# Kernel optimization log

Hardware: AMD Instinct MI355X
Metric: run time of the kernel (lower is better)

Reference implementation:

```python
import jax, jax.numpy as jnp
import numpy as np

NUM_HEADS = 4
NUM_GROUPS = 32
EPS = 1e-5


def setup_inputs() -> dict:
    key = jax.random.key(0)
    ks = jax.random.split(key, 4)
    ch = 256
    x = jax.random.normal(ks[0], (16, ch, 32, 32), dtype=jnp.float32)
    gn_w = jnp.ones((ch,), jnp.float32)
    gn_b = jnp.zeros((ch,), jnp.float32)
    # conv1x1 weights, kaiming-ish scale
    qkv_w = jax.random.normal(ks[1], (3 * ch, ch), dtype=jnp.float32) / np.sqrt(ch)
    qkv_b = jnp.zeros((3 * ch,), jnp.float32)
    proj_w = jax.random.normal(ks[2], (ch, ch), dtype=jnp.float32) / np.sqrt(ch)
    proj_b = jnp.zeros((ch,), jnp.float32)
    return {"x": x, "gn_w": gn_w, "gn_b": gn_b, "qkv_w": qkv_w,
            "qkv_b": qkv_b, "proj_w": proj_w, "proj_b": proj_b}


def _group_norm(x, w, b):
    bsz, c, h, wd = x.shape
    g = NUM_GROUPS
    xg = x.reshape(bsz, g, c // g, h, wd)
    mean = xg.mean(axis=(2, 3, 4), keepdims=True)
    var = xg.var(axis=(2, 3, 4), keepdims=True)
    xg = (xg - mean) * jax.lax.rsqrt(var + EPS)
    return xg.reshape(bsz, c, h, wd) * w[None, :, None, None] + b[None, :, None, None]


def reference(x, gn_w, gn_b, qkv_w, qkv_b, proj_w, proj_b):
    b, c, h, w = x.shape
    hd = c // NUM_HEADS
    scale = hd ** (-0.5)
    y = _group_norm(x, gn_w, gn_b)
    # 1x1 conv == channel matmul
    qkv = jnp.einsum('oc,bchw->bohw', qkv_w, y) + qkv_b[None, :, None, None]
    q, k, v = jnp.split(qkv, 3, axis=1)
    q = q.reshape(b, NUM_HEADS, hd, h * w)
    k = k.reshape(b, NUM_HEADS, hd, h * w)
    v = v.reshape(b, NUM_HEADS, hd, h * w)
    attn = jnp.einsum('bhdi,bhdj->bhij', q * scale, k)
    attn = jax.nn.softmax(attn, axis=-1)
    out = jnp.einsum('bhij,bhdj->bhdi', attn, v)
    out = out.reshape(b, c, h, w)
    out = jnp.einsum('oc,bchw->bohw', proj_w, out) + proj_b[None, :, None, None]
    return x + out
```

## Files before the change

kernel.cpp:

```cpp
#include <hip/hip_runtime.h>
#include <cstddef>

#define B_   16
#define C_   256
#define HW_  1024
#define NH_  4
#define NG_  32
#define CPG_ 8
#define CS_  0.18033688f

typedef __attribute__((ext_vector_type(8))) short bf16x8;
typedef __attribute__((ext_vector_type(4))) short s16x4;
typedef __attribute__((ext_vector_type(8))) _Float16 f16x8;
typedef __attribute__((ext_vector_type(4))) float f32x4;

#define MFMA16B(a, b, c) __builtin_amdgcn_mfma_f32_16x16x32_bf16(a, b, c, 0, 0, 0)
#define MFMA16H(a, b, c) __builtin_amdgcn_mfma_f32_16x16x32_f16(a, b, c, 0, 0, 0)

#if __has_builtin(__builtin_amdgcn_mfma_f32_16x16x16bf16_1k)
#define HAVE_MFMA16K16 1
#define MFMA16B4(a, b, c) __builtin_amdgcn_mfma_f32_16x16x16bf16_1k(a, b, c, 0, 0, 0)
#else
#define HAVE_MFMA16K16 0
#endif

__device__ __forceinline__ float bf2f(unsigned short h) {
    unsigned int u = ((unsigned int)h) << 16;
    return __builtin_bit_cast(float, u);
}
__device__ __forceinline__ unsigned short f2bf(float f) {
    unsigned int u = __builtin_bit_cast(unsigned int, f);
    u += 0x7FFFu + ((u >> 16) & 1u);
    return (unsigned short)(u >> 16);
}
__device__ __forceinline__ unsigned packbf(float a, float b) {
    unsigned ua = __builtin_bit_cast(unsigned, a) + 0x8000u;
    unsigned ub = __builtin_bit_cast(unsigned, b) + 0x8000u;
    return __builtin_amdgcn_perm(ub, ua, 0x07060302u);
}
__device__ __forceinline__ unsigned pkh(float a, float b) {
    auto h2 = __builtin_amdgcn_cvt_pkrtz(a, b);
    return __builtin_bit_cast(unsigned, h2);
}

__global__ __launch_bounds__(256) void wcvt_kernel(
    const float* __restrict__ qw, const float* __restrict__ pw,
    unsigned short* __restrict__ oq, unsigned short* __restrict__ op)
{
    int i = blockIdx.x * 256 + threadIdx.x;
    const float* s; unsigned short* d; int j;
    if (i < 49152) { s = qw; d = oq; j = i; }
    else           { s = pw; d = op; j = i - 49152; }
    float4 f = ((const float4*)s)[j];
    uint2 u = {pkh(f.x, f.y), pkh(f.z, f.w)};
    *(uint2*)&d[(size_t)j * 4] = u;
}

__global__ __launch_bounds__(256) void gn_kernel(
    const float* __restrict__ x,
    const float* __restrict__ gw,
    const float* __restrict__ gb,
    float2* __restrict__ scsh)
{
    int blk = blockIdx.x;
    const float* xg = x + (size_t)blk * CPG_ * HW_;
    const int N = CPG_ * HW_;

    float s = 0.f, ss = 0.f;
    for (int e = threadIdx.x * 4; e < N; e += 1024) {
        float4 v4 = *(const float4*)&xg[e];
        s  += v4.x + v4.y + v4.z + v4.w;
        ss += v4.x * v4.x + v4.y * v4.y + v4.z * v4.z + v4.w * v4.w;
    }
    #pragma unroll
    for (int off = 32; off > 0; off >>= 1) {
        s  += __shfl_down(s, off, 64);
        ss += __shfl_down(ss, off, 64);
    }
    __shared__ float red[8];
    __shared__ float2 stf;
    int lane = threadIdx.x & 63, wv = threadIdx.x >> 6;
    if (lane == 0) { red[wv] = s; red[4 + wv] = ss; }
    __syncthreads();
    if (threadIdx.x == 0) {
        float S  = red[0] + red[1] + red[2] + red[3];
        float SS = red[4] + red[5] + red[6] + red[7];
        float mean = S / (float)N;
        float var  = SS / (float)N - mean * mean;
        stf = make_float2(mean, rsqrtf(var + 1e-5f));
    }
    __syncthreads();
    if (threadIdx.x < 8) {
        int ch = (blk & 31) * CPG_ + threadIdx.x;
        float sc = stf.y * gw[ch];
        float sh = gb[ch] - stf.x * sc;
        scsh[blk * 8 + threadIdx.x] = make_float2(sc, sh);
    }
}

template <bool FUSE_GN, bool FINAL>
__global__ __launch_bounds__(256) void gemm_mfma_kernel(
    const unsigned short* __restrict__ W16,
    const float* __restrict__ Xf,
    const unsigned short* __restrict__ OP,
    const float* __restrict__ LPp,
    const float* __restrict__ bias,
    const float2* __restrict__ scsh,
    const float* __restrict__ res,
    float* __restrict__ outF,
    unsigned short* __restrict__ qT,
    unsigned short* __restrict__ kT,
    unsigned short* __restrict__ vN,
    int M, int K, int N)
{
    __shared__ union {
        struct { unsigned short A[2][128][40]; unsigned short Bt[2][64][40]; } st;
        unsigned short nd[2][64][72];
        unsigned short mn[128][72];
    } L;

    const int b  = blockIdx.z;
    const int m0 = blockIdx.y * 128, n0 = blockIdx.x * 64;
    const int t  = threadIdx.x;
    const int l15 = t & 15, quad = (t >> 4) & 3;
    const int wave = t >> 6, wm = wave >> 1, wn = wave & 1;

    union HF { uint4 q; f16x8 v; };

    f32x4 acc[4][2];
    #pragma unroll
    for (int mt = 0; mt < 4; ++mt)
        #pragma unroll
        for (int nt = 0; nt < 2; ++nt)
            acc[mt][nt] = (f32x4){0.f, 0.f, 0.f, 0.f};

    const int ar = t >> 1, akh = (t & 1) * 16;
    const int bn = t & 63, bkb = t >> 6;

    float rinv[4];
    if (FINAL) {
        int n = n0 + bn;
        #pragma unroll
        for (int h = 0; h < 4; ++h) {
            float l0 = LPp[(size_t)(b * 4 + h) * 1024 + n];
            float l1 = LPp[(size_t)(64 + b * 4 + h) * 1024 + n];
            rinv[h] = 1.f / (l0 + l1);
        }
    }

    uint4 pa0, pa1;
    float pv[8];
    unsigned short ph0[8], ph1[8];
    int   pH = 0;
    float2 ss[8];

    auto PREF = [&](int k0) {
        const unsigned short* wp = &W16[(size_t)(m0 + ar) * K + k0 + akh];
        pa0 = *(const uint4*)wp;
        pa1 = *(const uint4*)(wp + 8);
        int ch = k0 + bkb * 8;
        if (FINAL) {
            pH = ch >> 6;
            size_t base = ((size_t)(b * 4 + pH) * 64 + (ch & 63)) * 1024 + n0 + bn;
            #pragma unroll
            for (int j = 0; j < 8; ++j) {
                ph0[j] = OP[base + (size_t)j * 1024];
                ph1[j] = OP[(size_t)64 * 64 * 1024 + base + (size_t)j * 1024];
            }
        } else {
            const float* xp = &Xf[((size_t)b * K + ch) * N + n0 + bn];
            #pragma unroll
            for (int j = 0; j < 8; ++j) pv[j] = xp[(size_t)j * N];
            if (FUSE_GN) {
                const float4* sp = (const float4*)&scsh[b * C_ + ch];
                #pragma unroll
                for (int q2 = 0; q2 < 4; ++q2) ((float4*)ss)[q2] = sp[q2];
            }
        }
    };

    PREF(0);
    const int NIT = K / 32;
    for (int it = 0; it < NIT; ++it) {
        const int bsel = it & 1;
        *(uint4*)&L.st.A[bsel][ar][akh]     = pa0;
        *(uint4*)&L.st.A[bsel][ar][akh + 8] = pa1;
        {
            float v[8];
            if (FINAL) {
                float ri = rinv[pH];
                #pragma unroll
                for (int j = 0; j < 8; ++j)
                    v[j] = (bf2f(ph0[j]) + bf2f(ph1[j])) * ri;
            } else {
                #pragma unroll
                for (int j = 0; j < 8; ++j) v[j] = pv[j];
                if (FUSE_GN) {
                    #pragma unroll
                    for (int j = 0; j < 8; ++j) v[j] = v[j] * ss[j].x + ss[j].y;
                }
            }
            uint4 bw = {pkh(v[0], v[1]), pkh(v[2], v[3]), pkh(v[4], v[5]), pkh(v[6], v[7])};
            *(uint4*)&L.st.Bt[bsel][bn][bkb * 8] = bw;
        }
        __syncthreads();
        if (it + 1 < NIT) PREF((it + 1) * 32);
        HF af[4], bfv[2];
        #pragma unroll
        for (int mt = 0; mt < 4; ++mt)
            af[mt].q = *(const uint4*)&L.st.A[bsel][wm * 64 + mt * 16 + l15][quad * 8];
        #pragma unroll
        for (int nt = 0; nt < 2; ++nt)
            bfv[nt].q = *(const uint4*)&L.st.Bt[bsel][wn * 32 + nt * 16 + l15][quad * 8];
        #pragma unroll
        for (int mt = 0; mt < 4; ++mt)
            #pragma unroll
            for (int nt = 0; nt < 2; ++nt)
                acc[mt][nt] = MFMA16H(af[mt].v, bfv[nt].v, acc[mt][nt]);
    }
    __syncthreads();

    if (FINAL) {
        #pragma unroll
        for (int mt = 0; mt < 4; ++mt) {
            #pragma unroll
            for (int rr = 0; rr < 4; ++rr) {
                int m = m0 + wm * 64 + mt * 16 + quad * 4 + rr;
                float bv = bias[m];
                #pragma unroll
                for (int nt = 0; nt < 2; ++nt) {
                    int n = n0 + wn * 32 + nt * 16 + l15;
                    size_t off = ((size_t)b * M + m) * (size_t)N + n;
                    outF[off] = acc[mt][nt][rr] + bv + res[off];
                }
            }
        }
    } else if (m0 < 512) {
        const float qsc = (m0 < 256) ? CS_ : 1.f;
        #pragma unroll
        for (int mt = 0; mt < 4; ++mt)
            #pragma unroll
            for (int rr = 0; rr < 4; ++rr) {
                int dl = mt * 16 + quad * 4 + rr;
                float bv = bias[m0 + wm * 64 + dl];
                #pragma unroll
                for (int nt = 0; nt < 2; ++nt)
                    L.nd[wm][wn * 32 + nt * 16 + l15][dl] = f2bf((acc[mt][nt][rr] + bv) * qsc);
            }
        __syncthreads();
        unsigned short* dst = (m0 < 256) ? qT : kT;
        int headbase = (m0 & 255) >> 6;
        int hl = t >> 7, tt = t & 127;
        int nl = tt >> 1, db = (tt & 1) * 32;
        const unsigned short* src = &L.nd[hl][nl][db];
        unsigned short* gp = &dst[(((size_t)(b * 4 + headbase + hl)) * 1024 + n0 + nl) * 64 + db];
        uint4 u0 = *(const uint4*)(src);
        uint4 u1 = *(const uint4*)(src + 8);
        uint4 u2 = *(const uint4*)(src + 16);
        uint4 u3 = *(const uint4*)(src + 24);
        *(uint4*)(gp)      = u0;
        *(uint4*)(gp + 8)  = u1;
        *(uint4*)(gp + 16) = u2;
        *(uint4*)(gp + 24) = u3;
    } else {
        #pragma unroll
        for (int mt = 0; mt < 4; ++mt)
            #pragma unroll
            for (int rr = 0; rr < 4; ++rr) {
                int ml = wm * 64 + mt * 16 + quad * 4 + rr;
                float bv = bias[m0 + ml];
                #pragma unroll
                for (int nt = 0; nt < 2; ++nt)
                    L.mn[ml][wn * 32 + nt * 16 + l15] = f2bf(acc[mt][nt][rr] + bv);
            }
        __syncthreads();
        int ml = t & 127, nb = t >> 7;
        const unsigned short* src = &L.mn[ml][nb * 32];
        unsigned short* gp = &vN[((size_t)b * 256 + (m0 - 512) + ml) * 1024 + n0 + nb * 32];
        uint4 u0 = *(const uint4*)(src);
        uint4 u1 = *(const uint4*)(src + 8);
        uint4 u2 = *(const uint4*)(src + 16);
        uint4 u3 = *(const uint4*)(src + 24);
        *(uint4*)(gp)      = u0;
        *(uint4*)(gp + 8)  = u1;
        *(uint4*)(gp + 16) = u2;
        *(uint4*)(gp + 24) = u3;
    }
}

__global__ __launch_bounds__(256) void attn_mfma_kernel(
    const unsigned short* __restrict__ qT,
    const unsigned short* __restrict__ kT,
    const unsigned short* __restrict__ vN,
    unsigned short* __restrict__ OP,
    float* __restrict__ LP)
{
    __shared__ unsigned short Kt[2][64][72];
    __shared__ unsigned short Vs[2][64][72];

    const int t    = threadIdx.x;
    const int wv   = t >> 6;
    const int l15  = t & 15;
    const int quad = (t >> 4) & 3;
    const int bh   = blockIdx.x;
    const int i0   = blockIdx.y * 128;
    const int jh   = blockIdx.z;

    union FragU { uint4 q; unsigned u[4]; bf16x8 v; };

    FragU qf[2][2];
    {
        const unsigned short* qg = qT + (size_t)bh * (1024 * 64);
        int qrow = i0 + wv * 32 + l15;
        #pragma unroll
        for (int nt = 0; nt < 2; ++nt)
            #pragma unroll
            for (int kt = 0; kt < 2; ++kt)
                qf[nt][kt].q = *(const uint4*)&qg[(size_t)(qrow + nt * 16) * 64 + kt * 32 + quad * 8];
    }

    f32x4 accO[4][2];
    #pragma unroll
    for (int m = 0; m < 4; ++m)
        #pragma unroll
        for (int n = 0; n < 2; ++n)
            accO[m][n] = (f32x4){0.f, 0.f, 0.f, 0.f};
    float l_i[2] = {0.f, 0.f};
#if HAVE_MFMA16K16
    f32x4 accL[2] = {(f32x4){0.f, 0.f, 0.f, 0.f}, (f32x4){0.f, 0.f, 0.f, 0.f}};
    const s16x4 ones4 = {(short)0x3F80, (short)0x3F80, (short)0x3F80, (short)0x3F80};
#endif

    const unsigned short* kg = kT + (size_t)bh * (1024 * 64);
    const unsigned short* vg = vN + (size_t)bh * (64 * 1024);

    const int slbase = l15 + ((quad & 1) << 5);
    const bool upper = (t & 32) != 0;
    (void)slbase; (void)upper;
    const int sr = t >> 2, sc = (t & 3) * 16;

    uint4 kr0, kr1, vr0, vr1;
    {
        const int j0 = jh * 512;
        const unsigned short* kp = &kg[(size_t)(j0 + sr) * 64 + sc];
        const unsigned short* vp = &vg[(size_t)sr * 1024 + j0 + sc];
        kr0 = *(const uint4*)kp;  kr1 = *(const uint4*)(kp + 8);
        vr0 = *(const uint4*)vp;  vr1 = *(const uint4*)(vp + 8);
    }

    for (int it = 0; it < 8; ++it) {
        const int bsel = it & 1;
        *(uint4*)&Kt[bsel][sr][sc]     = kr0;
        *(uint4*)&Kt[bsel][sr][sc + 8] = kr1;
        *(uint4*)&Vs[bsel][sr][sc]     = vr0;
        *(uint4*)&Vs[bsel][sr][sc + 8] = vr1;
        __syncthreads();
        if (it < 7) {
            const int j0n = jh * 512 + (it + 1) * 64;
            const unsigned short* kp = &kg[(size_t)(j0n + sr) * 64 + sc];
            const unsigned short* vp = &vg[(size_t)sr * 1024 + j0n + sc];
            kr0 = *(const uint4*)kp;  kr1 = *(const uint4*)(kp + 8);
            vr0 = *(const uint4*)vp;  vr1 = *(const uint4*)(vp + 8);
        }

        f32x4 accS[4][2];
        #pragma unroll
        for (int mt = 0; mt < 4; ++mt) {
            FragU ak[2];
            #pragma unroll
            for (int kt = 0; kt < 2; ++kt)
                ak[kt].q = *(const uint4*)&Kt[bsel][mt * 16 + l15][kt * 32 + quad * 8];
            #pragma unroll
            for (int nt = 0; nt < 2; ++nt) {
                f32x4 z = (f32x4){0.f, 0.f, 0.f, 0.f};
                z = MFMA16B(ak[0].v, qf[nt][0].v, z);
                z = MFMA16B(ak[1].v, qf[nt][1].v, z);
                accS[mt][nt] = z;
            }
        }

#if HAVE_MFMA16K16
        union PB { unsigned u[2]; s16x4 v; };
        PB pb[4][2];
        #pragma unroll
        for (int mt = 0; mt < 4; ++mt)
            #pragma unroll
            for (int nt = 0; nt < 2; ++nt) {
                float p0 = exp2f(accS[mt][nt][0]);
                float p1 = exp2f(accS[mt][nt][1]);
                float p2 = exp2f(accS[mt][nt][2]);
                float p3 = exp2f(accS[mt][nt][3]);
                pb[mt][nt].u[0] = packbf(p0, p1);
                pb[mt][nt].u[1] = packbf(p2, p3);
            }
        #pragma unroll
        for (int mt = 0; mt < 4; ++mt)
            #pragma unroll
            for (int nt = 0; nt < 2; ++nt)
                accL[nt] = MFMA16B4(ones4, pb[mt][nt].v, accL[nt]);
        #pragma unroll
        for (int mtd = 0; mtd < 4; ++mtd) {
            union AV { uint2 d; s16x4 v; } av[4];
            #pragma unroll
            for (int mt = 0; mt < 4; ++mt)
                av[mt].d = *(const uint2*)&Vs[bsel][mtd * 16 + l15][mt * 16 + quad * 4];
            #pragma unroll
            for (int nt = 0; nt < 2; ++nt)
                #pragma unroll
                for (int mt = 0; mt < 4; ++mt)
                    accO[mtd][nt] = MFMA16B4(av[mt].v, pb[mt][nt].v, accO[mtd][nt]);
        }
#else
        float rs[2] = {0.f, 0.f};
        unsigned pk[4][2][2];
        #pragma unroll
        for (int mt = 0; mt < 4; ++mt)
            #pragma unroll
            for (int nt = 0; nt < 2; ++nt) {
                float p0 = exp2f(accS[mt][nt][0]);
                float p1 = exp2f(accS[mt][nt][1]);
                float p2 = exp2f(accS[mt][nt][2]);
                float p3 = exp2f(accS[mt][nt][3]);
                rs[nt] += (p0 + p1) + (p2 + p3);
                pk[mt][nt][0] = packbf(p0, p1);
                pk[mt][nt][1] = packbf(p2, p3);
            }
        #pragma unroll
        for (int nt = 0; nt < 2; ++nt) {
            float r = rs[nt];
            r += __shfl_xor(r, 16, 64);
            r += __shfl_xor(r, 32, 64);
            l_i[nt] += r;
        }
        FragU bfr[2][2];
        #pragma unroll
        for (int kt = 0; kt < 2; ++kt)
            #pragma unroll
            for (int nt = 0; nt < 2; ++nt)
                #pragma unroll
                for (int w4 = 0; w4 < 4; ++w4) {
                    int sl = slbase + ((w4 >> 1) << 4);
                    int lo = __shfl((int)pk[2 * kt + 0][nt][w4 & 1], sl, 64);
                    int hi = __shfl((int)pk[2 * kt + 1][nt][w4 & 1], sl, 64);
                    bfr[kt][nt].u[w4] = (unsigned)(upper ? hi : lo);
                }
        #pragma unroll
        for (int mtd = 0; mtd < 4; ++mtd) {
            FragU av[2];
            #pragma unroll
            for (int kt = 0; kt < 2; ++kt)
                av[kt].q = *(const uint4*)&Vs[bsel][mtd * 16 + l15][kt * 32 + quad * 8];
            #pragma unroll
            for (int nt = 0; nt < 2; ++nt) {
                accO[mtd][nt] = MFMA16B(av[0].v, bfr[0][nt].v, accO[mtd][nt]);
                accO[mtd][nt] = MFMA16B(av[1].v, bfr[1][nt].v, accO[mtd][nt]);
            }
        }
#endif
    }

#if HAVE_MFMA16K16
    l_i[0] = accL[0][0];
    l_i[1] = accL[1][0];
#endif

    unsigned short* ob = OP + ((size_t)jh * 64 + bh) * (64 * 1024) + i0 + wv * 32;
    #pragma unroll
    for (int mtd = 0; mtd < 4; ++mtd)
        #pragma unroll
        for (int nt = 0; nt < 2; ++nt)
            #pragma unroll
            for (int rr = 0; rr < 4; ++rr) {
                int d = mtd * 16 + quad * 4 + rr;
                ob[(size_t)d * 1024 + nt * 16 + l15] = f2bf(accO[mtd][nt][rr]);
            }
    if (quad == 0) {
        float* lp = &LP[((size_t)jh * 64 + bh) * 1024 + i0 + wv * 32 + l15];
        lp[0]  = l_i[0];
        lp[16] = l_i[1];
    }
}

extern "C" void kernel_launch(void* const* d_in, const int* in_sizes, int n_in,
                              void* d_out, int out_size, void* d_ws, size_t ws_size,
                              hipStream_t stream)
{
    const float* x      = (const float*)d_in[0];
    const float* gn_w   = (const float*)d_in[1];
    const float* gn_b   = (const float*)d_in[2];
    const float* qkv_w  = (const float*)d_in[3];
    const float* qkv_b  = (const float*)d_in[4];
    const float* proj_w = (const float*)d_in[5];
    const float* proj_b = (const float*)d_in[6];
    float* out = (float*)d_out;

    char* ws = (char*)d_ws;
    float2* scsh = (float2*)ws;
    unsigned short* w16q = (unsigned short*)(ws + 32768);
    unsigned short* w16p = w16q + 768 * 256;
    unsigned short* qT   = w16p + 256 * 256;
    unsigned short* kT   = qT + (size_t)B_ * NH_ * HW_ * 64;
    unsigned short* vN   = kT + (size_t)B_ * NH_ * HW_ * 64;
    unsigned short* OP   = vN + (size_t)B_ * C_ * HW_;
    float*          LP   = (float*)(OP + (size_t)2 * B_ * C_ * HW_);
    (void)in_sizes; (void)n_in; (void)out_size; (void)ws_size;

    wcvt_kernel<<<dim3(256), 256, 0, stream>>>(qkv_w, proj_w, w16q, w16p);
    gn_kernel<<<dim3(B_ * NG_), 256, 0, stream>>>(x, gn_w, gn_b, scsh);

    gemm_mfma_kernel<true, false><<<dim3(HW_ / 64, (3 * C_) / 128, B_), 256, 0, stream>>>(
        w16q, x, nullptr, nullptr, qkv_b, scsh, nullptr, nullptr,
        qT, kT, vN, 3 * C_, C_, HW_);

    attn_mfma_kernel<<<dim3(NH_ * B_, HW_ / 128, 2), 256, 0, stream>>>(qT, kT, vN, OP, LP);

    gemm_mfma_kernel<false, true><<<dim3(HW_ / 64, C_ / 128, B_), 256, 0, stream>>>(
        w16p, nullptr, OP, LP, proj_b, nullptr, x, out,
        nullptr, nullptr, nullptr, C_, C_, HW_);
}
```

Before: 149.7 us.

## Merge GN and weight-convert launches, split GEMM kernels, retile projection to 64x64

The weight-conversion and group-norm-stats kernels become one launch, with block index selecting the role, which removes one kernel launch. The templated GEMM is split into dedicated QKV and projection kernels with hardcoded sizes and non-unrolled K loops. The projection kernel now uses 64x64 tiles instead of 128x64, doubling its grid to 1024 blocks and cutting per-thread accumulators to raise occupancy on the small M=256 GEMM. packbf uses a hardware bf16 convert builtin when one exists.

Result: no change. 149.5 us (-0.1%).

```diff
diff --git a/kernel.cpp b/kernel.cpp
--- a/kernel.cpp
+++ b/kernel.cpp
@@ -33,35 +33,41 @@
     u += 0x7FFFu + ((u >> 16) & 1u);
     return (unsigned short)(u >> 16);
 }
+#if __has_builtin(__builtin_amdgcn_cvt_pk_bf16_f32)
+__device__ __forceinline__ unsigned packbf(float a, float b) {
+    auto v = __builtin_amdgcn_cvt_pk_bf16_f32(a, b);
+    return __builtin_bit_cast(unsigned, v);
+}
+#else
 __device__ __forceinline__ unsigned packbf(float a, float b) {
     unsigned ua = __builtin_bit_cast(unsigned, a) + 0x8000u;
     unsigned ub = __builtin_bit_cast(unsigned, b) + 0x8000u;
     return __builtin_amdgcn_perm(ub, ua, 0x07060302u);
 }
+#endif
 __device__ __forceinline__ unsigned pkh(float a, float b) {
     auto h2 = __builtin_amdgcn_cvt_pkrtz(a, b);
     return __builtin_bit_cast(unsigned, h2);
 }
 
-__global__ __launch_bounds__(256) void wcvt_kernel(
+__global__ __launch_bounds__(256) void gn_wcvt_kernel(
+    const float* __restrict__ x,
+    const float* __restrict__ gw,
+    const float* __restrict__ gb,
+    float2* __restrict__ scsh,
     const float* __restrict__ qw, const float* __restrict__ pw,
     unsigned short* __restrict__ oq, unsigned short* __restrict__ op)
 {
-    int i = blockIdx.x * 256 + threadIdx.x;
-    const float* s; unsigned short* d; int j;
-    if (i < 49152) { s = qw; d = oq; j = i; }
-    else           { s = pw; d = op; j = i - 49152; }
-    float4 f = ((const float4*)s)[j];
-    uint2 u = {pkh(f.x, f.y), pkh(f.z, f.w)};
-    *(uint2*)&d[(size_t)j * 4] = u;
-}
-
-__global__ __launch_bounds__(256) void gn_kernel(
-    const float* __restrict__ x,
-    const float* __restrict__ gw,
-    const float* __restrict__ gb,
-    float2* __restrict__ scsh)
-{
+    if (blockIdx.x >= 512) {
+        int i = (blockIdx.x - 512) * 256 + threadIdx.x;
+        const float* s; unsigned short* d; int j;
+        if (i < 49152) { s = qw; d = oq; j = i; }
+        else           { s = pw; d = op; j = i - 49152; }
+        float4 f = ((const float4*)s)[j];
+        uint2 u = {pkh(f.x, f.y), pkh(f.z, f.w)};
+        *(uint2*)&d[(size_t)j * 4] = u;
+        return;
+    }
     int blk = blockIdx.x;
     const float* xg = x + (size_t)blk * CPG_ * HW_;
     const int N = CPG_ * HW_;
@@ -98,21 +104,16 @@
     }
 }
 
-template <bool FUSE_GN, bool FINAL>
-__global__ __launch_bounds__(256) void gemm_mfma_kernel(
+__global__ __launch_bounds__(256) void qkv_mfma_kernel(
     const unsigned short* __restrict__ W16,
     const float* __restrict__ Xf,
-    const unsigned short* __restrict__ OP,
-    const float* __restrict__ LPp,
     const float* __restrict__ bias,
     const float2* __restrict__ scsh,
-    const float* __restrict__ res,
-    float* __restrict__ outF,
     unsigned short* __restrict__ qT,
     unsigned short* __restrict__ kT,
-    unsigned short* __restrict__ vN,
-    int M, int K, int N)
+    unsigned short* __restrict__ vN)
 {
+    const int M = 768, K = 256, N = 1024;
     __shared__ union {
         struct { unsigned short A[2][128][40]; unsigned short Bt[2][64][40]; } st;
         unsigned short nd[2][64][72];
@@ -137,21 +138,8 @@
     const int ar = t >> 1, akh = (t & 1) * 16;
     const int bn = t & 63, bkb = t >> 6;
 
-    float rinv[4];
-    if (FINAL) {
-        int n = n0 + bn;
-        #pragma unroll
-        for (int h = 0; h < 4; ++h) {
-            float l0 = LPp[(size_t)(b * 4 + h) * 1024 + n];
-            float l1 = LPp[(size_t)(64 + b * 4 + h) * 1024 + n];
-            rinv[h] = 1.f / (l0 + l1);
-        }
-    }
-
     uint4 pa0, pa1;
     float pv[8];
-    unsigned short ph0[8], ph1[8];
-    int   pH = 0;
     float2 ss[8];
 
     auto PREF = [&](int k0) {
@@ -159,52 +147,29 @@
         pa0 = *(const uint4*)wp;
         pa1 = *(const uint4*)(wp + 8);
         int ch = k0 + bkb * 8;
-        if (FINAL) {
-            pH = ch >> 6;
-            size_t base = ((size_t)(b * 4 + pH) * 64 + (ch & 63)) * 1024 + n0 + bn;
-            #pragma unroll
-            for (int j = 0; j < 8; ++j) {
-                ph0[j] = OP[base + (size_t)j * 1024];
-                ph1[j] = OP[(size_t)64 * 64 * 1024 + base + (size_t)j * 1024];
-            }
-        } else {
-            const float* xp = &Xf[((size_t)b * K + ch) * N + n0 + bn];
-            #pragma unroll
-            for (int j = 0; j < 8; ++j) pv[j] = xp[(size_t)j * N];
-            if (FUSE_GN) {
-                const float4* sp = (const float4*)&scsh[b * C_ + ch];
-                #pragma unroll
-                for (int q2 = 0; q2 < 4; ++q2) ((float4*)ss)[q2] = sp[q2];
-            }
-        }
+        const float* xp = &Xf[((size_t)b * K + ch) * N + n0 + bn];
+        #pragma unroll
+        for (int j = 0; j < 8; ++j) pv[j] = xp[(size_t)j * N];
+        const float4* sp = (const float4*)&scsh[b * C_ + ch];
+        #pragma unroll
+        for (int q2 = 0; q2 < 4; ++q2) ((float4*)ss)[q2] = sp[q2];
     };
 
     PREF(0);
-    const int NIT = K / 32;
-    for (int it = 0; it < NIT; ++it) {
+    #pragma unroll 1
+    for (int it = 0; it < 8; ++it) {
         const int bsel = it & 1;
         *(uint4*)&L.st.A[bsel][ar][akh]     = pa0;
         *(uint4*)&L.st.A[bsel][ar][akh + 8] = pa1;
         {
             float v[8];
-            if (FINAL) {
-                float ri = rinv[pH];
-                #pragma unroll
-                for (int j = 0; j < 8; ++j)
-                    v[j] = (bf2f(ph0[j]) + bf2f(ph1[j])) * ri;
-            } else {
-                #pragma unroll
-                for (int j = 0; j < 8; ++j) v[j] = pv[j];
-                if (FUSE_GN) {
-                    #pragma unroll
-                    for (int j = 0; j < 8; ++j) v[j] = v[j] * ss[j].x + ss[j].y;
-                }
-            }
+            #pragma unroll
+            for (int j = 0; j < 8; ++j) v[j] = pv[j] * ss[j].x + ss[j].y;
             uint4 bw = {pkh(v[0], v[1]), pkh(v[2], v[3]), pkh(v[4], v[5]), pkh(v[6], v[7])};
             *(uint4*)&L.st.Bt[bsel][bn][bkb * 8] = bw;
         }
         __syncthreads();
-        if (it + 1 < NIT) PREF((it + 1) * 32);
+        if (it + 1 < 8) PREF((it + 1) * 32);
         HF af[4], bfv[2];
         #pragma unroll
         for (int mt = 0; mt < 4; ++mt)
@@ -220,22 +185,7 @@
     }
     __syncthreads();
 
-    if (FINAL) {
-        #pragma unroll
-        for (int mt = 0; mt < 4; ++mt) {
-            #pragma unroll
-            for (int rr = 0; rr < 4; ++rr) {
-                int m = m0 + wm * 64 + mt * 16 + quad * 4 + rr;
-                float bv = bias[m];
-                #pragma unroll
-                for (int nt = 0; nt < 2; ++nt) {
-                    int n = n0 + wn * 32 + nt * 16 + l15;
-                    size_t off = ((size_t)b * M + m) * (size_t)N + n;
-                    outF[off] = acc[mt][nt][rr] + bv + res[off];
-                }
-            }
-        }
-    } else if (m0 < 512) {
+    if (m0 < 512) {
         const float qsc = (m0 < 256) ? CS_ : 1.f;
         #pragma unroll
         for (int mt = 0; mt < 4; ++mt)
@@ -288,6 +238,108 @@
     }
 }
 
+__global__ __launch_bounds__(256) void proj_mfma_kernel(
+    const unsigned short* __restrict__ W16,
+    const unsigned short* __restrict__ OP,
+    const float* __restrict__ LPp,
+    const float* __restrict__ bias,
+    const float* __restrict__ res,
+    float* __restrict__ outF)
+{
+    const int M = 256, K = 256, N = 1024;
+    __shared__ struct { unsigned short A[2][64][40]; unsigned short Bt[2][64][40]; } L;
+
+    const int b  = blockIdx.z;
+    const int m0 = blockIdx.y * 64, n0 = blockIdx.x * 64;
+    const int t  = threadIdx.x;
+    const int l15 = t & 15, quad = (t >> 4) & 3;
+    const int wave = t >> 6, wm = wave >> 1, wn = wave & 1;
+
+    union HF { uint4 q; f16x8 v; };
+
+    f32x4 acc[2][2];
+    #pragma unroll
+    for (int mt = 0; mt < 2; ++mt)
+        #pragma unroll
+        for (int nt = 0; nt < 2; ++nt)
+            acc[mt][nt] = (f32x4){0.f, 0.f, 0.f, 0.f};
+
+    const int ar = t >> 2, akh = (t & 3) * 8;
+    const int bn = t & 63, bkb = t >> 6;
+
+    float rinv[4];
+    {
+        int n = n0 + bn;
+        #pragma unroll
+        for (int h = 0; h < 4; ++h) {
+            float l0 = LPp[(size_t)(b * 4 + h) * 1024 + n];
+            float l1 = LPp[(size_t)(64 + b * 4 + h) * 1024 + n];
+            rinv[h] = 1.f / (l0 + l1);
+        }
+    }
+
+    uint4 pa;
+    unsigned short ph0[8], ph1[8];
+    int pH = 0;
+
+    auto PREF = [&](int k0) {
+        pa = *(const uint4*)&W16[(size_t)(m0 + ar) * K + k0 + akh];
+        int ch = k0 + bkb * 8;
+        pH = ch >> 6;
+        size_t base = ((size_t)(b * 4 + pH) * 64 + (ch & 63)) * 1024 + n0 + bn;
+        #pragma unroll
+        for (int j = 0; j < 8; ++j) {
+            ph0[j] = OP[base + (size_t)j * 1024];
+            ph1[j] = OP[(size_t)64 * 64 * 1024 + base + (size_t)j * 1024];
+        }
+    };
+
+    PREF(0);
+    #pragma unroll 1
+    for (int it = 0; it < 8; ++it) {
+        const int bsel = it & 1;
+        *(uint4*)&L.A[bsel][ar][akh] = pa;
+        {
+            float ri = rinv[pH];
+            float v[8];
+            #pragma unroll
+            for (int j = 0; j < 8; ++j)
+                v[j] = (bf2f(ph0[j]) + bf2f(ph1[j])) * ri;
+            uint4 bw = {pkh(v[0], v[1]), pkh(v[2], v[3]), pkh(v[4], v[5]), pkh(v[6], v[7])};
+            *(uint4*)&L.Bt[bsel][bn][bkb * 8] = bw;
+        }
+        __syncthreads();
+        if (it + 1 < 8) PREF((it + 1) * 32);
+        HF af[2], bfv[2];
+        #pragma unroll
+        for (int mt = 0; mt < 2; ++mt)
+            af[mt].q = *(const uint4*)&L.A[bsel][wm * 32 + mt * 16 + l15][quad * 8];
+        #pragma unroll
+        for (int nt = 0; nt < 2; ++nt)
+            bfv[nt].q = *(const uint4*)&L.Bt[bsel][wn * 32 + nt * 16 + l15][quad * 8];
+        #pragma unroll
+        for (int mt = 0; mt < 2; ++mt)
+            #pragma unroll
+            for (int nt = 0; nt < 2; ++nt)
+                acc[mt][nt] = MFMA16H(af[mt].v, bfv[nt].v, acc[mt][nt]);
+    }
+
+    #pragma unroll
+    for (int mt = 0; mt < 2; ++mt) {
+        #pragma unroll
+        for (int rr = 0; rr < 4; ++rr) {
+            int m = m0 + wm * 32 + mt * 16 + quad * 4 + rr;
+            float bv = bias[m];
+            #pragma unroll
+            for (int nt = 0; nt < 2; ++nt) {
+                int n = n0 + wn * 32 + nt * 16 + l15;
+                size_t off = ((size_t)b * M + m) * (size_t)N + n;
+                outF[off] = acc[mt][nt][rr] + bv + res[off];
+            }
+        }
+    }
+}
+
 __global__ __launch_bounds__(256) void attn_mfma_kernel(
     const unsigned short* __restrict__ qT,
     const unsigned short* __restrict__ kT,
@@ -505,16 +557,14 @@
     float*          LP   = (float*)(OP + (size_t)2 * B_ * C_ * HW_);
     (void)in_sizes; (void)n_in; (void)out_size; (void)ws_size;
 
-    wcvt_kernel<<<dim3(256), 256, 0, stream>>>(qkv_w, proj_w, w16q, w16p);
-    gn_kernel<<<dim3(B_ * NG_), 256, 0, stream>>>(x, gn_w, gn_b, scsh);
-
-    gemm_mfma_kernel<true, false><<<dim3(HW_ / 64, (3 * C_) / 128, B_), 256, 0, stream>>>(
-        w16q, x, nullptr, nullptr, qkv_b, scsh, nullptr, nullptr,
-        qT, kT, vN, 3 * C_, C_, HW_);
+    gn_wcvt_kernel<<<dim3(768), 256, 0, stream>>>(
+        x, gn_w, gn_b, scsh, qkv_w, proj_w, w16q, w16p);
+
+    qkv_mfma_kernel<<<dim3(HW_ / 64, 6, B_), 256, 0, stream>>>(
+        w16q, x, qkv_b, scsh, qT, kT, vN);
 
     attn_mfma_kernel<<<dim3(NH_ * B_, HW_ / 128, 2), 256, 0, stream>>>(qT, kT, vN, OP, LP);
 
-    gemm_mfma_kernel<false, true><<<dim3(HW_ / 64, C_ / 128, B_), 256, 0, stream>>>(
-        w16p, nullptr, OP, LP, proj_b, nullptr, x, out,
-        nullptr, nullptr, nullptr, C_, C_, HW_);
-}
+    proj_mfma_kernel<<<dim3(HW_ / 64, C_ / 64, B_), 256, 0, stream>>>(
+        w16p, OP, LP, proj_b, x, out);
+}
```
